# Kernel tuning notes

Hardware: AMD Instinct MI355X
Metric: run time of the kernel (lower is better)

The kernel has to match this reference:

```python
import jax, jax.numpy as jnp
import numpy as np

ALPHA = 0.2        # LeakyReLU slope inside attention layers
OUT_SLOPE = 0.01   # F.leaky_relu default slope on the final output
EPS = 1e-16        # guards isolated nodes (pyGAT divides by rowsum directly)


def _sp_layer(x, src, dst, W, a, concat, n_nodes):
    # x: [N, F_in], W: [F_in, F_out], a: [2*F_out]
    h = x @ W                                            # [N, F_out]
    eh = jnp.concatenate([h[src], h[dst]], axis=1)       # [E, 2*F_out]
    e = jnp.exp(-jax.nn.leaky_relu(eh @ a, ALPHA))       # [E] unnormalized attn
    denom = jax.ops.segment_sum(e, src, num_segments=n_nodes)          # [N]
    agg = jax.ops.segment_sum(e[:, None] * h[dst], src, num_segments=n_nodes)  # [N, F_out]
    hp = agg / (denom[:, None] + EPS)
    return jax.nn.elu(hp) if concat else hp


def _forward_one(xb, eib, W_heads, a_heads, W_out, a_out):
    n = xb.shape[0]
    src, dst = eib[0], eib[1]
    # independent heads (static small loop), concat on feature dim
    heads = [_sp_layer(xb, src, dst, W_heads[h], a_heads[h], True, n)
             for h in range(W_heads.shape[0])]
    xc = jnp.concatenate(heads, axis=1)                  # [N, nheads*nhid]
    out = _sp_layer(xc, src, dst, W_out, a_out, False, n)  # [N, nclass]
    return jax.nn.leaky_relu(out, OUT_SLOPE)


def setup_inputs() -> dict:
    key = jax.random.key(0)
    B, N, E = 8, 10000, 160000
    nfeat, nhid, nclass, nheads = 256, 64, 64, 8
    ks = jax.random.split(key, 6)
    x = jax.random.normal(ks[0], (B, N, nfeat), dtype=jnp.float32)
    edge_index = jax.random.randint(ks[1], (B, 2, E), 0, N, dtype=jnp.int32)
    # xavier-normal-ish init scales
    W_heads = jax.random.normal(ks[2], (nheads, nfeat, nhid), dtype=jnp.float32) * np.sqrt(2.0 / (nfeat + nhid))
    a_heads = jax.random.normal(ks[3], (nheads, 2 * nhid), dtype=jnp.float32) * np.sqrt(2.0 / (2 * nhid + 1))
    W_out = jax.random.normal(ks[4], (nheads * nhid, nclass), dtype=jnp.float32) * np.sqrt(2.0 / (nheads * nhid + nclass))
    a_out = jax.random.normal(ks[5], (2 * nclass,), dtype=jnp.float32) * np.sqrt(2.0 / (2 * nclass + 1))
    return {"x": x, "edge_index": edge_index, "W_heads": W_heads,
            "a_heads": a_heads, "W_out": W_out, "a_out": a_out, "batch_size": B}


def reference(x, edge_index, W_heads, a_heads, W_out, a_out, batch_size):
    # batch loop in the original is a pure map over graphs -> vmap
    return jax.vmap(lambda xb, eib: _forward_one(xb, eib, W_heads, a_heads, W_out, a_out))(x, edge_index)
```

## Files before the change

### kernel.cpp

```cpp
#include <hip/hip_runtime.h>
#include <cstdint>
#include <cstddef>

#define NND   10000
#define NED   160000
#define NB    8
#define NF    256
#define NHID  64
#define HEADS 8
#define F1    512
#define NCLS  64

#define QSH   10
#define NQ    10
#define NK    (NND * NQ)
#define CHNK  1024
#define NCH   ((NK + CHNK - 1) / CHNK)

#define ALPHA_SLOPE 0.2f
#define OUT_SLOPE   0.01f
#define EPS         1e-16f

typedef unsigned short u16;
typedef short short8 __attribute__((ext_vector_type(8)));
typedef float f32x4 __attribute__((ext_vector_type(4)));

static const size_t B_WCHI = 0;
static const size_t B_WCLO = 262144;
static const size_t B_WOHI = 524288;
static const size_t B_WOLO = 589824;
static const size_t B_AS1  = 655360;
static const size_t B_AD1  = 3215360;
static const size_t B_AS2  = 5775360;
static const size_t B_AD2  = 6095360;
static const size_t B_CNT  = 6415360;
static const size_t B_CUR  = 9615360;
static const size_t B_ROWS = 12815360;
static const size_t B_BSUM = 13135424;
static const size_t B_DST  = 13151808;
static const size_t B_SCR  = 15711808;
#define ZSTRU 16000000ull
static const size_t S_PERZ = 2 * ZSTRU;

__device__ __forceinline__ u16 f32_to_bf16_rn(float f) {
  uint32_t u = __float_as_uint(f);
  uint32_t r = u + 0x7fffu + ((u >> 16) & 1u);
  return (u16)(r >> 16);
}
__device__ __forceinline__ float bf16_to_f32(u16 s) {
  return __uint_as_float((uint32_t)s << 16);
}
__device__ __forceinline__ void split1(float v, u16& h, u16& l) {
  h = f32_to_bf16_rn(v);
  float r = v - bf16_to_f32(h);
  l = f32_to_bf16_rn(r);
}

__global__ __launch_bounds__(256) void k_wsplit1(const float* __restrict__ Whd,
                                                 u16* __restrict__ hi,
                                                 u16* __restrict__ lo) {
  int t = blockIdx.x * 256 + threadIdx.x;
  int lane = t & 63;
  int frag = t >> 6;
  int nj = frag & 3;
  int wq = (frag >> 2) & 3;
  int ts = (frag >> 4) & 7;
  int by = frag >> 7;
  int lm = lane & 15, lkg = lane >> 4;
  int n = by * 256 + wq * 64 + nj * 16 + lm;
  int h = n >> 6, nc = n & 63;
  u16 hv[8], lv[8];
#pragma unroll
  for (int j = 0; j < 8; ++j) {
    int k = ts * 32 + lkg * 8 + j;
    split1(Whd[h * (NF * NHID) + k * NHID + nc], hv[j], lv[j]);
  }
  size_t o = (size_t)t * 8;
  *(ushort4*)(hi + o) = make_ushort4(hv[0], hv[1], hv[2], hv[3]);
  *(ushort4*)(hi + o + 4) = make_ushort4(hv[4], hv[5], hv[6], hv[7]);
  *(ushort4*)(lo + o) = make_ushort4(lv[0], lv[1], lv[2], lv[3]);
  *(ushort4*)(lo + o + 4) = make_ushort4(lv[4], lv[5], lv[6], lv[7]);
}

__global__ __launch_bounds__(256) void k_wsplit2(const float* __restrict__ Wo,
                                                 u16* __restrict__ hi,
                                                 u16* __restrict__ lo) {
  int t = blockIdx.x * 256 + threadIdx.x;
  int lane = t & 63;
  int frag = t >> 6;
  int nj = frag & 3, ts = frag >> 2;
  int lm = lane & 15, lkg = lane >> 4;
  int n = nj * 16 + lm;
  u16 hv[8], lv[8];
#pragma unroll
  for (int j = 0; j < 8; ++j) {
    int k = ts * 32 + lkg * 8 + j;
    split1(Wo[k * NCLS + n], hv[j], lv[j]);
  }
  size_t o = (size_t)t * 8;
  *(ushort4*)(hi + o) = make_ushort4(hv[0], hv[1], hv[2], hv[3]);
  *(ushort4*)(hi + o + 4) = make_ushort4(hv[4], hv[5], hv[6], hv[7]);
  *(ushort4*)(lo + o) = make_ushort4(lv[0], lv[1], lv[2], lv[3]);
  *(ushort4*)(lo + o + 4) = make_ushort4(lv[4], lv[5], lv[6], lv[7]);
}

__global__ __launch_bounds__(512) void k_gemm1(
    const float* __restrict__ x,
    const u16* __restrict__ Bfh, const u16* __restrict__ Bfl,
    u16* __restrict__ h1_s,
    const float* __restrict__ avec,
    float* __restrict__ as_g, float* __restrict__ ad_g,
    int base_b, int zsh) {
  __shared__ u16 As_hi[64][40];
  __shared__ u16 As_lo[64][40];

  const int zmask = (1 << zsh) - 1;
  const int z = blockIdx.x & zmask;
  const int wg = blockIdx.x >> zsh;
  const int b = base_b + z;
  const float* A = x + (size_t)b * NND * NF;
  u16* C = h1_s + (size_t)z * ZSTRU;
  float* as_ = as_g + (size_t)b * NND * 8;
  float* ad_ = ad_g + (size_t)b * NND * 8;

  const int m0 = wg * 64;
  const int tid = threadIdx.x;
  const int lane = tid & 63;
  const int w = tid >> 6;
  const int lm = lane & 15;
  const int lkg = lane >> 4;
  const int by = w >> 2, wq = w & 3;

  f32x4 acc[4][4];
#pragma unroll
  for (int mi = 0; mi < 4; ++mi)
#pragma unroll
    for (int nj = 0; nj < 4; ++nj) acc[mi][nj] = 0.f;

  for (int t = 0; t < 8; ++t) {
    const int kk = t * 32;
    __syncthreads();
    {
      int rr = tid >> 3, kf = (tid & 7) * 4;
      int gm = m0 + rr;
      float4 v = make_float4(0.f, 0.f, 0.f, 0.f);
      if (gm < NND) v = *(const float4*)(A + (size_t)gm * NF + kk + kf);
      ushort4 hv, lv;
      split1(v.x, hv.x, lv.x); split1(v.y, hv.y, lv.y);
      split1(v.z, hv.z, lv.z); split1(v.w, hv.w, lv.w);
      *(ushort4*)&As_hi[rr][kf] = hv;
      *(ushort4*)&As_lo[rr][kf] = lv;
    }
    short8 bh[4], bl[4];
    {
      size_t fb = (((size_t)(by * 8 + t) * 4 + wq) * 4) * 512 + (size_t)lane * 8;
#pragma unroll
      for (int nj = 0; nj < 4; ++nj) {
        bh[nj] = *(const short8*)(Bfh + fb + nj * 512);
        bl[nj] = *(const short8*)(Bfl + fb + nj * 512);
      }
    }
    __syncthreads();

    short8 ah[4], al[4];
#pragma unroll
    for (int mi = 0; mi < 4; ++mi) {
      int row = mi * 16 + lm;
      ah[mi] = *(const short8*)&As_hi[row][lkg * 8];
      al[mi] = *(const short8*)&As_lo[row][lkg * 8];
    }
#pragma unroll
    for (int mi = 0; mi < 4; ++mi)
#pragma unroll
      for (int nj = 0; nj < 4; ++nj) {
        acc[mi][nj] = __builtin_amdgcn_mfma_f32_16x16x32_bf16(ah[mi], bh[nj], acc[mi][nj], 0, 0, 0);
        acc[mi][nj] = __builtin_amdgcn_mfma_f32_16x16x32_bf16(ah[mi], bl[nj], acc[mi][nj], 0, 0, 0);
        acc[mi][nj] = __builtin_amdgcn_mfma_f32_16x16x32_bf16(al[mi], bh[nj], acc[mi][nj], 0, 0, 0);
      }
  }

  const int hb = w;
  const int n0 = w * 64;
  float a_sv[4], a_dv[4];
#pragma unroll
  for (int nj = 0; nj < 4; ++nj) {
    a_sv[nj] = avec[hb * 128 + nj * 16 + lm];
    a_dv[nj] = avec[hb * 128 + 64 + nj * 16 + lm];
  }
#pragma unroll
  for (int mi = 0; mi < 4; ++mi) {
#pragma unroll
    for (int rr = 0; rr < 4; ++rr) {
      int gm = m0 + mi * 16 + lkg * 4 + rr;
      float ps = acc[mi][0][rr] * a_sv[0] + acc[mi][1][rr] * a_sv[1] +
                 acc[mi][2][rr] * a_sv[2] + acc[mi][3][rr] * a_sv[3];
      float pd = acc[mi][0][rr] * a_dv[0] + acc[mi][1][rr] * a_dv[1] +
                 acc[mi][2][rr] * a_dv[2] + acc[mi][3][rr] * a_dv[3];
#pragma unroll
      for (int off = 1; off < 16; off <<= 1) {
        ps += __shfl_xor(ps, off, 16);
        pd += __shfl_xor(pd, off, 16);
      }
      if (gm < NND) {
#pragma unroll
        for (int nj = 0; nj < 4; ++nj)
          C[(size_t)gm * F1 + n0 + nj * 16 + lm] = f32_to_bf16_rn(acc[mi][nj][rr]);
        if (lm == 0) {
          as_[(size_t)gm * 8 + hb] = ps;
          ad_[(size_t)gm * 8 + hb] = pd;
        }
      }
    }
  }
}

__global__ __launch_bounds__(256) void k_gemm2(
    const u16* __restrict__ Ahi_s, const u16* __restrict__ Alo_s,
    const u16* __restrict__ Bfh, const u16* __restrict__ Bfl,
    u16* __restrict__ C_s,
    const float* __restrict__ avec,
    float* __restrict__ as_g, float* __restrict__ ad_g,
    int base_b, int zsh) {
  __shared__ u16 As_hi[64][40];
  __shared__ u16 As_lo[64][40];

  const int zmask = (1 << zsh) - 1;
  const int z = blockIdx.x & zmask;
  const int wg = blockIdx.x >> zsh;
  const int b = base_b + z;
  const u16* Ahi = Ahi_s + (size_t)z * ZSTRU;
  const u16* Alo = Alo_s + (size_t)z * ZSTRU;
  u16* C = C_s + (size_t)z * ZSTRU;
  float* as_ = as_g + (size_t)b * NND;
  float* ad_ = ad_g + (size_t)b * NND;

  const int tid = threadIdx.x;
  const int lane = tid & 63;
  const int w = tid >> 6;
  const int lm = lane & 15;
  const int lkg = lane >> 4;
  const int m0 = wg * 64;

  f32x4 acc[4];
#pragma unroll
  for (int j = 0; j < 4; ++j) acc[j] = 0.f;

  for (int ts = 0; ts < 16; ++ts) {
    const int kk = ts * 32;
    __syncthreads();
#pragma unroll
    for (int u = 0; u < 2; ++u) {
      int e = u * 256 + tid;
      int rr = e >> 3, kf = (e & 7) * 4;
      int gm = m0 + rr;
      ushort4 hv = make_ushort4(0, 0, 0, 0), lv = make_ushort4(0, 0, 0, 0);
      if (gm < NND) {
        size_t g = (size_t)gm * F1 + kk + kf;
        hv = *(const ushort4*)(Ahi + g);
        lv = *(const ushort4*)(Alo + g);
      }
      *(ushort4*)&As_hi[rr][kf] = hv;
      *(ushort4*)&As_lo[rr][kf] = lv;
    }
    short8 bh[4], bl[4];
    {
      size_t fb = (size_t)(ts * 4) * 512 + (size_t)lane * 8;
#pragma unroll
      for (int nj = 0; nj < 4; ++nj) {
        bh[nj] = *(const short8*)(Bfh + fb + nj * 512);
        bl[nj] = *(const short8*)(Bfl + fb + nj * 512);
      }
    }
    __syncthreads();

    short8 ah, al;
    {
      int row = w * 16 + lm;
      ah = *(const short8*)&As_hi[row][lkg * 8];
      al = *(const short8*)&As_lo[row][lkg * 8];
    }
#pragma unroll
    for (int nj = 0; nj < 4; ++nj) {
      acc[nj] = __builtin_amdgcn_mfma_f32_16x16x32_bf16(ah, bh[nj], acc[nj], 0, 0, 0);
      acc[nj] = __builtin_amdgcn_mfma_f32_16x16x32_bf16(ah, bl[nj], acc[nj], 0, 0, 0);
      acc[nj] = __builtin_amdgcn_mfma_f32_16x16x32_bf16(al, bh[nj], acc[nj], 0, 0, 0);
    }
  }

  float a_sv[4], a_dv[4];
#pragma unroll
  for (int nj = 0; nj < 4; ++nj) {
    a_sv[nj] = avec[nj * 16 + lm];
    a_dv[nj] = avec[64 + nj * 16 + lm];
  }
#pragma unroll
  for (int rr = 0; rr < 4; ++rr) {
    int gm = m0 + w * 16 + lkg * 4 + rr;
    float ps = acc[0][rr] * a_sv[0] + acc[1][rr] * a_sv[1] +
               acc[2][rr] * a_sv[2] + acc[3][rr] * a_sv[3];
    float pd = acc[0][rr] * a_dv[0] + acc[1][rr] * a_dv[1] +
               acc[2][rr] * a_dv[2] + acc[3][rr] * a_dv[3];
#pragma unroll
    for (int off = 1; off < 16; off <<= 1) {
      ps += __shfl_xor(ps, off, 16);
      pd += __shfl_xor(pd, off, 16);
    }
    if (gm < NND) {
#pragma unroll
      for (int nj = 0; nj < 4; ++nj)
        C[(size_t)gm * NCLS + nj * 16 + lm] = f32_to_bf16_rn(acc[nj][rr]);
      if (lm == 0) {
        as_[gm] = ps;
        ad_[gm] = pd;
      }
    }
  }
}


__global__ __launch_bounds__(256) void k_hist(const int* __restrict__ ei,
                                              int* __restrict__ counts) {
  int z = blockIdx.x & 7;
  int blk = blockIdx.x >> 3;
  int e = blk * 256 + threadIdx.x;
  if (e < NED) {
    int s = ei[(size_t)z * 2 * NED + e];
    int d = ei[(size_t)z * 2 * NED + NED + e];
    atomicAdd(&counts[(size_t)z * NK + s * NQ + (d >> QSH)], 1);
  }
}

__global__ __launch_bounds__(256) void k_psum(const int* __restrict__ counts,
                                              int* __restrict__ bsum) {
  __shared__ int lds[256];
  int b = blockIdx.x & 7;
  int c = blockIdx.x >> 3;
  const int* cb = counts + (size_t)b * NK + c * CHNK;
  int rem = NK - c * CHNK;
  int i4 = threadIdx.x * 4;
  int s = 0;
  if (i4 + 3 < rem) {
    int4 v = *(const int4*)(cb + i4);
    s = v.x + v.y + v.z + v.w;
  } else {
    for (int j = 0; j < 4; ++j) if (i4 + j < rem) s += cb[i4 + j];
  }
  lds[threadIdx.x] = s;
  __syncthreads();
  for (int off = 128; off; off >>= 1) {
    if (threadIdx.x < off) lds[threadIdx.x] += lds[threadIdx.x + off];
    __syncthreads();
  }
  if (threadIdx.x == 0) bsum[b * NCH + c] = lds[0];
}

__global__ __launch_bounds__(1024) void k_bscan(int* __restrict__ bsum) {
  __shared__ int lds[8][128];
  int b = threadIdx.x >> 7;
  int j = threadIdx.x & 127;
  int v = (j < NCH) ? bsum[b * NCH + j] : 0;
  lds[b][j] = v;
  __syncthreads();
  for (int off = 1; off < 128; off <<= 1) {
    int t = (j >= off) ? lds[b][j - off] : 0;
    __syncthreads();
    lds[b][j] += t;
    __syncthreads();
  }
  if (j < NCH) bsum[b * NCH + j] = lds[b][j] - v;
}

__global__ __launch_bounds__(256) void k_apply(const int* __restrict__ counts,
                                               const int* __restrict__ bsum,
                                               int* __restrict__ cursor,
                                               int* __restrict__ rows) {
  __shared__ int lds[256];
  int b = blockIdx.x & 7;
  int c = blockIdx.x >> 3;
  const int* cb = counts + (size_t)b * NK + c * CHNK;
  int* cu = cursor + (size_t)b * NK + c * CHNK;
  int* rb = rows + b * (NND + 1);
  int rem = NK - c * CHNK;
  int i4 = threadIdx.x * 4;
  int v[4];
  int s = 0;
#pragma unroll
  for (int j = 0; j < 4; ++j) {
    v[j] = (i4 + j < rem) ? cb[i4 + j] : 0;
    s += v[j];
  }
  lds[threadIdx.x] = s;
  __syncthreads();
  for (int off = 1; off < 256; off <<= 1) {
    int t = (threadIdx.x >= off) ? lds[threadIdx.x - off] : 0;
    __syncthreads();
    lds[threadIdx.x] += t;
    __syncthreads();
  }
  int run = bsum[b * NCH + c] + lds[threadIdx.x] - s;
#pragma unroll
  for (int j = 0; j < 4; ++j) {
    int i = i4 + j;
    if (i < rem) {
      cu[i] = run;
      int gk = c * CHNK + i;
      if (gk % NQ == 0) {
        int n = gk / NQ;
        if (n < NND) rb[n] = run;
      }
      run += v[j];
    }
  }
  if (c == 0 && threadIdx.x == 0) rb[NND] = NED;
}

__global__ __launch_bounds__(256) void k_scatter(const int* __restrict__ ei,
                                                 int* __restrict__ cursor,
                                                 u16* __restrict__ dst_s) {
  int z = blockIdx.x & 7;
  int blk = blockIdx.x >> 3;
  int e = blk * 256 + threadIdx.x;
  if (e < NED) {
    int s = ei[(size_t)z * 2 * NED + e];
    int d = ei[(size_t)z * 2 * NED + NED + e];
    int pos = atomicAdd(&cursor[(size_t)z * NK + s * NQ + (d >> QSH)], 1);
    dst_s[(size_t)z * NED + pos] = (u16)d;
  }
}

#define UPK8(q, e) do { \
  acc[0] = fmaf(e, __uint_as_float((q).x << 16), acc[0]); \
  acc[1] = fmaf(e, __uint_as_float((q).x & 0xffff0000u), acc[1]); \
  acc[2] = fmaf(e, __uint_as_float((q).y << 16), acc[2]); \
  acc[3] = fmaf(e, __uint_as_float((q).y & 0xffff0000u), acc[3]); \
  acc[4] = fmaf(e, __uint_as_float((q).z << 16), acc[4]); \
  acc[5] = fmaf(e, __uint_as_float((q).z & 0xffff0000u), acc[5]); \
  acc[6] = fmaf(e, __uint_as_float((q).w << 16), acc[6]); \
  acc[7] = fmaf(e, __uint_as_float((q).w & 0xffff0000u), acc[7]); \
} while (0)

#define LKY(t) ((t) >= 0.f ? (t) : ALPHA_SLOPE * (t))

__global__ __launch_bounds__(256) void k_agg1(
    const int* __restrict__ rows_g, const u16* __restrict__ dst_g,
    const u16* __restrict__ h1_s,
    const float* __restrict__ as_g, const float* __restrict__ ad_g,
    u16* __restrict__ xchi_s, u16* __restrict__ xclo_s,
    int base_b, int zsh) {
  const int zmask = (1 << zsh) - 1;
  const int z = blockIdx.x & zmask;
  const int idx = blockIdx.x >> zsh;
  const int b = base_b + z;
  const int* rows = rows_g + (size_t)b * (NND + 1);
  const u16* dst = dst_g + (size_t)b * NED;
  const u16* h1 = h1_s + (size_t)z * ZSTRU;
  const float* as_ = as_g + (size_t)b * NND * 8;
  const float* ad_ = ad_g + (size_t)b * NND * 8;
  u16* xh = xchi_s + (size_t)z * ZSTRU;
  u16* xl = xclo_s + (size_t)z * ZSTRU;

  int lane = threadIdx.x & 63;
  int n = (idx * 256 + threadIdx.x) >> 6;
  if (n >= NND) return;
  const int hh = lane >> 3;
  const float asv = as_[n * 8 + hh];
  int beg = rows[n], end = rows[n + 1];
  float acc[8] = {};
  float den = 0.f;
  int i = beg;
  for (; i + 4 <= end; i += 4) {
    int d0 = dst[i], d1 = dst[i + 1], d2 = dst[i + 2], d3 = dst[i + 3];
    float t0 = LKY(asv + ad_[d0 * 8 + hh]);
    float t1 = LKY(asv + ad_[d1 * 8 + hh]);
    float t2 = LKY(asv + ad_[d2 * 8 + hh]);
    float t3 = LKY(asv + ad_[d3 * 8 + hh]);
    float e0 = __expf(-t0), e1 = __expf(-t1);
    float e2 = __expf(-t2), e3 = __expf(-t3);
    uint4 q0 = *((const uint4*)(h1 + (size_t)d0 * F1) + lane);
    uint4 q1 = *((const uint4*)(h1 + (size_t)d1 * F1) + lane);
    uint4 q2 = *((const uint4*)(h1 + (size_t)d2 * F1) + lane);
    uint4 q3 = *((const uint4*)(h1 + (size_t)d3 * F1) + lane);
    UPK8(q0, e0); UPK8(q1, e1); UPK8(q2, e2); UPK8(q3, e3);
    den += (e0 + e1) + (e2 + e3);
  }
  for (; i < end; ++i) {
    int d0 = dst[i];
    float t0 = LKY(asv + ad_[d0 * 8 + hh]);
    float e0 = __expf(-t0);
    uint4 q0 = *((const uint4*)(h1 + (size_t)d0 * F1) + lane);
    UPK8(q0, e0);
    den += e0;
  }
  float inv = 1.f / (den + EPS);
  u16 oh[8], ol[8];
#pragma unroll
  for (int j = 0; j < 8; ++j) {
    float v = acc[j] * inv;
    v = v > 0.f ? v : expm1f(v);
    split1(v, oh[j], ol[j]);
  }
  size_t wo = (size_t)n * F1 + lane * 8;
  *(ushort4*)(xh + wo) = make_ushort4(oh[0], oh[1], oh[2], oh[3]);
  *(ushort4*)(xh + wo + 4) = make_ushort4(oh[4], oh[5], oh[6], oh[7]);
  *(ushort4*)(xl + wo) = make_ushort4(ol[0], ol[1], ol[2], ol[3]);
  *(ushort4*)(xl + wo + 4) = make_ushort4(ol[4], ol[5], ol[6], ol[7]);
}

__global__ __launch_bounds__(256) void k_agg2(
    const int* __restrict__ rows_g, const u16* __restrict__ dst_g,
    const u16* __restrict__ h2_s,
    const float* __restrict__ as_g, const float* __restrict__ ad_g,
    float* __restrict__ out, int base_b, int zsh) {
  const int zmask = (1 << zsh) - 1;
  const int z = blockIdx.x & zmask;
  const int idx = blockIdx.x >> zsh;
  const int b = base_b + z;
  const int* rows = rows_g + (size_t)b * (NND + 1);
  const u16* dst = dst_g + (size_t)b * NED;
  const u16* h2 = h2_s + (size_t)z * ZSTRU;
  const float* as_ = as_g + (size_t)b * NND;
  const float* ad_ = ad_g + (size_t)b * NND;
  float* ob = out + (size_t)b * NND * NCLS;

  int lane = threadIdx.x & 63;
  int n = (idx * 256 + threadIdx.x) >> 6;
  if (n >= NND) return;
  const float asv = as_[n];
  int beg = rows[n], end = rows[n + 1];
  float acc = 0.f, den = 0.f;
  int i = beg;
  for (; i + 4 <= end; i += 4) {
    int d0 = dst[i], d1 = dst[i + 1], d2 = dst[i + 2], d3 = dst[i + 3];
    float t0 = LKY(asv + ad_[d0]);
    float t1 = LKY(asv + ad_[d1]);
    float t2 = LKY(asv + ad_[d2]);
    float t3 = LKY(asv + ad_[d3]);
    float e0 = __expf(-t0), e1 = __expf(-t1);
    float e2 = __expf(-t2), e3 = __expf(-t3);
    float h0 = bf16_to_f32(h2[(size_t)d0 * NCLS + lane]);
    float h1v = bf16_to_f32(h2[(size_t)d1 * NCLS + lane]);
    float h2v = bf16_to_f32(h2[(size_t)d2 * NCLS + lane]);
    float h3v = bf16_to_f32(h2[(size_t)d3 * NCLS + lane]);
    acc = fmaf(e0, h0, acc); acc = fmaf(e1, h1v, acc);
    acc = fmaf(e2, h2v, acc); acc = fmaf(e3, h3v, acc);
    den += (e0 + e1) + (e2 + e3);
  }
  for (; i < end; ++i) {
    int d0 = dst[i];
    float t0 = LKY(asv + ad_[d0]);
    float e0 = __expf(-t0);
    acc = fmaf(e0, bf16_to_f32(h2[(size_t)d0 * NCLS + lane]), acc);
    den += e0;
  }
  float v = acc / (den + EPS);
  ob[(size_t)n * NCLS + lane] = v >= 0.f ? v : OUT_SLOPE * v;
}

extern "C" void kernel_launch(void* const* d_in, const int* in_sizes, int n_in,
                              void* d_out, int out_size, void* d_ws, size_t ws_size,
                              hipStream_t stream) {
  const float* x       = (const float*)d_in[0];
  const int*   ei      = (const int*)d_in[1];
  const float* W_heads = (const float*)d_in[2];
  const float* a_heads = (const float*)d_in[3];
  const float* W_out   = (const float*)d_in[4];
  const float* a_out   = (const float*)d_in[5];
  float* out = (float*)d_out;

  char* base = (char*)d_ws;
  u16* wchi = (u16*)(base + B_WCHI);
  u16* wclo = (u16*)(base + B_WCLO);
  u16* wohi = (u16*)(base + B_WOHI);
  u16* wolo = (u16*)(base + B_WOLO);
  float* as1 = (float*)(base + B_AS1);
  float* ad1 = (float*)(base + B_AD1);
  float* as2 = (float*)(base + B_AS2);
  float* ad2 = (float*)(base + B_AD2);
  int* counts    = (int*)(base + B_CNT);
  int* cursor    = (int*)(base + B_CUR);
  int* rows      = (int*)(base + B_ROWS);
  int* bsum      = (int*)(base + B_BSUM);
  u16* dst_s     = (u16*)(base + B_DST);
  u16* scr       = (u16*)(base + B_SCR);

  int Z = 1, zsh = 0;
  if (ws_size >= B_SCR + 8 * S_PERZ) { Z = 8; zsh = 3; }
  else if (ws_size >= B_SCR + 4 * S_PERZ) { Z = 4; zsh = 2; }
  else if (ws_size >= B_SCR + 2 * S_PERZ) { Z = 2; zsh = 1; }

  u16* xchi = scr + 0;
  u16* xclo = scr + 5120000;
  u16* h1   = scr + 10240000;
  u16* h2   = scr + 15360000;

  k_wsplit1<<<64, 256, 0, stream>>>(W_heads, wchi, wclo);
  k_wsplit2<<<16, 256, 0, stream>>>(W_out, wohi, wolo);

  hipMemsetAsync(counts, 0, (size_t)NB * NK * sizeof(int), stream);
  k_hist<<<dim3(((NED + 255) / 256) * 8), 256, 0, stream>>>(ei, counts);
  k_psum<<<dim3(NCH * 8), 256, 0, stream>>>(counts, bsum);
  k_bscan<<<1, 1024, 0, stream>>>(bsum);
  k_apply<<<dim3(NCH * 8), 256, 0, stream>>>(counts, bsum, cursor, rows);
  k_scatter<<<dim3(((NED + 255) / 256) * 8), 256, 0, stream>>>(ei, cursor, dst_s);

  const int nwg = (NND + 63) / 64;
  for (int bb = 0; bb < NB; bb += Z) {
    k_gemm1<<<dim3(nwg << zsh), 512, 0, stream>>>(
        x, wchi, wclo, h1, a_heads, as1, ad1, bb, zsh);
    k_agg1<<<dim3(2500 << zsh), 256, 0, stream>>>(rows, dst_s, h1, as1, ad1,
                                                  xchi, xclo, bb, zsh);
    k_gemm2<<<dim3(nwg << zsh), 256, 0, stream>>>(
        xchi, xclo, wohi, wolo, h2, a_out, as2, ad2, bb, zsh);
    k_agg2<<<dim3(2500 << zsh), 256, 0, stream>>>(rows, dst_s, h2, as2, ad2,
                                                  out, bb, zsh);
  }
  (void)in_sizes; (void)n_in; (void)out_size;
}
```

Measured before the change: 448.0 us.

## Drop lo-part of layer-2 activations and bucket CSR by source only

The layer-1 aggregation now writes a single bf16 copy of the ELU output instead of a hi/lo split, and the second GEMM loads one A tile and runs two MFMAs per step instead of three. Separately, the CSR build no longer sub-buckets edges by destination range, so counts, scans and cursors shrink from N*10 to N entries per graph. This cuts memory traffic and MFMA work and lowers the workspace footprint, which may allow more graphs per batch pass. In exchange, layer-2 input precision falls to plain bf16, and neighbour order is no longer grouped by destination block, which may hurt gather locality.

```diff
diff --git a/kernel.cpp b/kernel.cpp
--- a/kernel.cpp
+++ b/kernel.cpp
@@ -11,11 +11,8 @@
 #define F1    512
 #define NCLS  64
 
-#define QSH   10
-#define NQ    10
-#define NK    (NND * NQ)
 #define CHNK  1024
-#define NCH   ((NK + CHNK - 1) / CHNK)
+#define NCH   10
 
 #define ALPHA_SLOPE 0.2f
 #define OUT_SLOPE   0.01f
@@ -34,12 +31,12 @@
 static const size_t B_AS2  = 5775360;
 static const size_t B_AD2  = 6095360;
 static const size_t B_CNT  = 6415360;
-static const size_t B_CUR  = 9615360;
-static const size_t B_ROWS = 12815360;
-static const size_t B_BSUM = 13135424;
-static const size_t B_DST  = 13151808;
-static const size_t B_SCR  = 15711808;
-#define ZSTRU 16000000ull
+static const size_t B_CUR  = 6735360;
+static const size_t B_ROWS = 7055360;
+static const size_t B_BSUM = 7375392;
+static const size_t B_DST  = 7375904;
+static const size_t B_SCR  = 9935936;
+#define ZSTRU 10880000ull
 static const size_t S_PERZ = 2 * ZSTRU;
 
 __device__ __forceinline__ u16 f32_to_bf16_rn(float f) {
@@ -215,21 +212,19 @@
 }
 
 __global__ __launch_bounds__(256) void k_gemm2(
-    const u16* __restrict__ Ahi_s, const u16* __restrict__ Alo_s,
+    const u16* __restrict__ A_s,
     const u16* __restrict__ Bfh, const u16* __restrict__ Bfl,
     u16* __restrict__ C_s,
     const float* __restrict__ avec,
     float* __restrict__ as_g, float* __restrict__ ad_g,
     int base_b, int zsh) {
-  __shared__ u16 As_hi[64][40];
-  __shared__ u16 As_lo[64][40];
+  __shared__ u16 As[64][40];
 
   const int zmask = (1 << zsh) - 1;
   const int z = blockIdx.x & zmask;
   const int wg = blockIdx.x >> zsh;
   const int b = base_b + z;
-  const u16* Ahi = Ahi_s + (size_t)z * ZSTRU;
-  const u16* Alo = Alo_s + (size_t)z * ZSTRU;
+  const u16* Ah = A_s + (size_t)z * ZSTRU;
   u16* C = C_s + (size_t)z * ZSTRU;
   float* as_ = as_g + (size_t)b * NND;
   float* ad_ = ad_g + (size_t)b * NND;
@@ -253,14 +248,9 @@
       int e = u * 256 + tid;
       int rr = e >> 3, kf = (e & 7) * 4;
       int gm = m0 + rr;
-      ushort4 hv = make_ushort4(0, 0, 0, 0), lv = make_ushort4(0, 0, 0, 0);
-      if (gm < NND) {
-        size_t g = (size_t)gm * F1 + kk + kf;
-        hv = *(const ushort4*)(Ahi + g);
-        lv = *(const ushort4*)(Alo + g);
-      }
-      *(ushort4*)&As_hi[rr][kf] = hv;
-      *(ushort4*)&As_lo[rr][kf] = lv;
+      ushort4 hv = make_ushort4(0, 0, 0, 0);
+      if (gm < NND) hv = *(const ushort4*)(Ah + (size_t)gm * F1 + kk + kf);
+      *(ushort4*)&As[rr][kf] = hv;
     }
     short8 bh[4], bl[4];
     {
@@ -273,17 +263,15 @@
     }
     __syncthreads();
 
-    short8 ah, al;
+    short8 ah;
     {
       int row = w * 16 + lm;
-      ah = *(const short8*)&As_hi[row][lkg * 8];
-      al = *(const short8*)&As_lo[row][lkg * 8];
+      ah = *(const short8*)&As[row][lkg * 8];
     }
 #pragma unroll
     for (int nj = 0; nj < 4; ++nj) {
       acc[nj] = __builtin_amdgcn_mfma_f32_16x16x32_bf16(ah, bh[nj], acc[nj], 0, 0, 0);
       acc[nj] = __builtin_amdgcn_mfma_f32_16x16x32_bf16(ah, bl[nj], acc[nj], 0, 0, 0);
-      acc[nj] = __builtin_amdgcn_mfma_f32_16x16x32_bf16(al, bh[nj], acc[nj], 0, 0, 0);
     }
   }
 
@@ -325,8 +313,7 @@
   int e = blk * 256 + threadIdx.x;
   if (e < NED) {
     int s = ei[(size_t)z * 2 * NED + e];
-    int d = ei[(size_t)z * 2 * NED + NED + e];
-    atomicAdd(&counts[(size_t)z * NK + s * NQ + (d >> QSH)], 1);
+    atomicAdd(&counts[z * NND + s], 1);
   }
 }
 
@@ -335,8 +322,8 @@
   __shared__ int lds[256];
   int b = blockIdx.x & 7;
   int c = blockIdx.x >> 3;
-  const int* cb = counts + (size_t)b * NK + c * CHNK;
-  int rem = NK - c * CHNK;
+  const int* cb = counts + (size_t)b * NND + c * CHNK;
+  int rem = NND - c * CHNK;
   int i4 = threadIdx.x * 4;
   int s = 0;
   if (i4 + 3 < rem) {
@@ -351,23 +338,23 @@
     if (threadIdx.x < off) lds[threadIdx.x] += lds[threadIdx.x + off];
     __syncthreads();
   }
-  if (threadIdx.x == 0) bsum[b * NCH + c] = lds[0];
-}
-
-__global__ __launch_bounds__(1024) void k_bscan(int* __restrict__ bsum) {
-  __shared__ int lds[8][128];
-  int b = threadIdx.x >> 7;
-  int j = threadIdx.x & 127;
-  int v = (j < NCH) ? bsum[b * NCH + j] : 0;
+  if (threadIdx.x == 0) bsum[b * 16 + c] = lds[0];
+}
+
+__global__ __launch_bounds__(128) void k_bscan(int* __restrict__ bsum) {
+  __shared__ int lds[8][16];
+  int b = threadIdx.x >> 4;
+  int j = threadIdx.x & 15;
+  int v = (j < NCH) ? bsum[b * 16 + j] : 0;
   lds[b][j] = v;
   __syncthreads();
-  for (int off = 1; off < 128; off <<= 1) {
+  for (int off = 1; off < 16; off <<= 1) {
     int t = (j >= off) ? lds[b][j - off] : 0;
     __syncthreads();
     lds[b][j] += t;
     __syncthreads();
   }
-  if (j < NCH) bsum[b * NCH + j] = lds[b][j] - v;
+  if (j < NCH) bsum[b * 16 + j] = lds[b][j] - v;
 }
 
 __global__ __launch_bounds__(256) void k_apply(const int* __restrict__ counts,
@@ -377,10 +364,10 @@
   __shared__ int lds[256];
   int b = blockIdx.x & 7;
   int c = blockIdx.x >> 3;
-  const int* cb = counts + (size_t)b * NK + c * CHNK;
-  int* cu = cursor + (size_t)b * NK + c * CHNK;
+  const int* cb = counts + (size_t)b * NND + c * CHNK;
+  int* cu = cursor + (size_t)b * NND + c * CHNK;
   int* rb = rows + b * (NND + 1);
-  int rem = NK - c * CHNK;
+  int rem = NND - c * CHNK;
   int i4 = threadIdx.x * 4;
   int v[4];
   int s = 0;
@@ -397,17 +384,13 @@
     lds[threadIdx.x] += t;
     __syncthreads();
   }
-  int run = bsum[b * NCH + c] + lds[threadIdx.x] - s;
+  int run = bsum[b * 16 + c] + lds[threadIdx.x] - s;
 #pragma unroll
   for (int j = 0; j < 4; ++j) {
     int i = i4 + j;
     if (i < rem) {
       cu[i] = run;
-      int gk = c * CHNK + i;
-      if (gk % NQ == 0) {
-        int n = gk / NQ;
-        if (n < NND) rb[n] = run;
-      }
+      rb[c * CHNK + i] = run;
       run += v[j];
     }
   }
@@ -423,7 +406,7 @@
   if (e < NED) {
     int s = ei[(size_t)z * 2 * NED + e];
     int d = ei[(size_t)z * 2 * NED + NED + e];
-    int pos = atomicAdd(&cursor[(size_t)z * NK + s * NQ + (d >> QSH)], 1);
+    int pos = atomicAdd(&cursor[z * NND + s], 1);
     dst_s[(size_t)z * NED + pos] = (u16)d;
   }
 }
@@ -445,7 +428,7 @@
     const int* __restrict__ rows_g, const u16* __restrict__ dst_g,
     const u16* __restrict__ h1_s,
     const float* __restrict__ as_g, const float* __restrict__ ad_g,
-    u16* __restrict__ xchi_s, u16* __restrict__ xclo_s,
+    u16* __restrict__ xc_s,
     int base_b, int zsh) {
   const int zmask = (1 << zsh) - 1;
   const int z = blockIdx.x & zmask;
@@ -456,8 +439,7 @@
   const u16* h1 = h1_s + (size_t)z * ZSTRU;
   const float* as_ = as_g + (size_t)b * NND * 8;
   const float* ad_ = ad_g + (size_t)b * NND * 8;
-  u16* xh = xchi_s + (size_t)z * ZSTRU;
-  u16* xl = xclo_s + (size_t)z * ZSTRU;
+  u16* xc = xc_s + (size_t)z * ZSTRU;
 
   int lane = threadIdx.x & 63;
   int n = (idx * 256 + threadIdx.x) >> 6;
@@ -492,18 +474,16 @@
     den += e0;
   }
   float inv = 1.f / (den + EPS);
-  u16 oh[8], ol[8];
+  u16 oh[8];
 #pragma unroll
   for (int j = 0; j < 8; ++j) {
     float v = acc[j] * inv;
     v = v > 0.f ? v : expm1f(v);
-    split1(v, oh[j], ol[j]);
+    oh[j] = f32_to_bf16_rn(v);
   }
   size_t wo = (size_t)n * F1 + lane * 8;
-  *(ushort4*)(xh + wo) = make_ushort4(oh[0], oh[1], oh[2], oh[3]);
-  *(ushort4*)(xh + wo + 4) = make_ushort4(oh[4], oh[5], oh[6], oh[7]);
-  *(ushort4*)(xl + wo) = make_ushort4(ol[0], ol[1], ol[2], ol[3]);
-  *(ushort4*)(xl + wo + 4) = make_ushort4(ol[4], ol[5], ol[6], ol[7]);
+  *(ushort4*)(xc + wo) = make_ushort4(oh[0], oh[1], oh[2], oh[3]);
+  *(ushort4*)(xc + wo + 4) = make_ushort4(oh[4], oh[5], oh[6], oh[7]);
 }
 
 __global__ __launch_bounds__(256) void k_agg2(
@@ -588,18 +568,17 @@
   else if (ws_size >= B_SCR + 4 * S_PERZ) { Z = 4; zsh = 2; }
   else if (ws_size >= B_SCR + 2 * S_PERZ) { Z = 2; zsh = 1; }
 
-  u16* xchi = scr + 0;
-  u16* xclo = scr + 5120000;
-  u16* h1   = scr + 10240000;
-  u16* h2   = scr + 15360000;
+  u16* xc = scr + 0;
+  u16* h1 = scr + 5120000;
+  u16* h2 = scr + 10240000;
 
   k_wsplit1<<<64, 256, 0, stream>>>(W_heads, wchi, wclo);
   k_wsplit2<<<16, 256, 0, stream>>>(W_out, wohi, wolo);
 
-  hipMemsetAsync(counts, 0, (size_t)NB * NK * sizeof(int), stream);
+  hipMemsetAsync(counts, 0, (size_t)NB * NND * sizeof(int), stream);
   k_hist<<<dim3(((NED + 255) / 256) * 8), 256, 0, stream>>>(ei, counts);
   k_psum<<<dim3(NCH * 8), 256, 0, stream>>>(counts, bsum);
-  k_bscan<<<1, 1024, 0, stream>>>(bsum);
+  k_bscan<<<1, 128, 0, stream>>>(bsum);
   k_apply<<<dim3(NCH * 8), 256, 0, stream>>>(counts, bsum, cursor, rows);
   k_scatter<<<dim3(((NED + 255) / 256) * 8), 256, 0, stream>>>(ei, cursor, dst_s);
 
@@ -608,9 +587,9 @@
     k_gemm1<<<dim3(nwg << zsh), 512, 0, stream>>>(
         x, wchi, wclo, h1, a_heads, as1, ad1, bb, zsh);
     k_agg1<<<dim3(2500 << zsh), 256, 0, stream>>>(rows, dst_s, h1, as1, ad1,
-                                                  xchi, xclo, bb, zsh);
+                                                  xc, bb, zsh);
     k_gemm2<<<dim3(nwg << zsh), 256, 0, stream>>>(
-        xchi, xclo, wohi, wolo, h2, a_out, as2, ad2, bb, zsh);
+        xc, wohi, wolo, h2, a_out, as2, ad2, bb, zsh);
     k_agg2<<<dim3(2500 << zsh), 256, 0, stream>>>(rows, dst_s, h2, as2, ad2,
                                                   out, bb, zsh);
   }
```

New measurement: 419.2 us. 1.07x faster.
